# Performance work log

Measured on AMD Instinct MI355X. Metric: run time of the kernel, lower is better.

Reference implementation:

```python
import jax, jax.numpy as jnp
import numpy as np

B, C, H, W = 32, 64, 56, 56
M, DIM, HEADS = 6, 192, 8
INNER = HEADS * C  # 512


def setup_inputs() -> dict:
    key = jax.random.key(0)
    ks = jax.random.split(key, 8)
    s = lambda fan: 1.0 / np.sqrt(fan)
    return {
        "x": jax.random.normal(ks[0], (B, C, H, W), jnp.float32),
        "z": jax.random.normal(ks[1], (B, M, DIM), jnp.float32),
        "Wk": jax.random.normal(ks[2], (DIM, INNER), jnp.float32) * s(DIM),
        "bk": jax.random.normal(ks[3], (INNER,), jnp.float32) * 0.01,
        "Wv": jax.random.normal(ks[4], (DIM, INNER), jnp.float32) * s(DIM),
        "bv": jax.random.normal(ks[5], (INNER,), jnp.float32) * 0.01,
        "Wo": jax.random.normal(ks[6], (INNER, C), jnp.float32) * s(INNER),
        "bo": jax.random.normal(ks[7], (C,), jnp.float32) * 0.01,
    }


def reference(x, z, Wk, bk, Wv, bv, Wo, bo):
    b, c, h, w = x.shape
    m = z.shape[1]
    heads = Wk.shape[1] // c
    scale = c ** (-0.5)
    # shared query: [b, hw, c] (broadcast over heads)
    q = x.reshape(b, c, h * w).transpose(0, 2, 1)
    # NOTE: original uses .view(b, heads, m, c) on [b, m, heads*c] -> pure reshape (no transpose)
    k = (z @ Wk + bk).reshape(b, heads, m, c)
    v = (z @ Wv + bv).reshape(b, heads, m, c)
    dots = jnp.einsum('bnc,bhmc->bhnm', q, k) * scale  # [b, heads, hw, m]
    attn = jax.nn.softmax(dots, axis=-1)
    out = jnp.einsum('bhnm,bhmc->bhnc', attn, v)       # [b, heads, hw, c]
    res = out.transpose(0, 2, 1, 3).reshape(b, h * w, heads * c)
    out = res @ Wo + bo                                 # [b, hw, c] (dropout: eval mode, identity)
    # NOTE: original does .view(b, c, h, w) on [b, hw, c] -> pure reshape (no transpose)
    out = out.reshape(b, c, h, w)
    return out + x
```

## Files before the change

kernel.cpp:

```cpp
#include <hip/hip_runtime.h>
#include <math.h>

#define NB 32
#define NC 64
#define NHW 3136
#define NM 6
#define NDIM 192
#define NHEADS 8
#define NINNER 512
#define NKV 3072
#define CHW (NC * NHW)
#define NG 48

__global__ __launch_bounds__(256) void kv_proj_kernel(
    const float* __restrict__ z, const float* __restrict__ Wk,
    const float* __restrict__ bk, const float* __restrict__ Wv,
    const float* __restrict__ bv, const float* __restrict__ Wo,
    float* __restrict__ kt, float* __restrict__ vw) {
  const int b = blockIdx.x;
  const int chunk = blockIdx.y;
  const int tid = threadIdx.x;
  const int idx = chunk * 256 + tid;
  const int mtok = chunk >> 1;
  const int i = idx & 511;

  __shared__ float vs[256];

  const float* __restrict__ zr = z + b * (NM * NDIM) + mtok * NDIM;

  float ak0 = bk[i], ak1 = 0.f, av0 = bv[i], av1 = 0.f;
  #pragma unroll 8
  for (int d = 0; d < NDIM; d += 2) {
    const float z0 = zr[d], z1 = zr[d + 1];
    ak0 = fmaf(z0, Wk[d * NINNER + i], ak0);
    ak1 = fmaf(z1, Wk[(d + 1) * NINNER + i], ak1);
    av0 = fmaf(z0, Wv[d * NINNER + i], av0);
    av1 = fmaf(z1, Wv[(d + 1) * NINNER + i], av1);
  }
  {
    const int h2 = idx / 384;
    const int mm2 = (idx >> 6) % 6;
    const int cc2 = idx & 63;
    kt[b * NKV + h2 * (NC * NM) + cc2 * NM + mm2] = ak0 + ak1;
  }
  vs[tid] = av0 + av1;
  __syncthreads();

  const int gl = tid >> 6;
  const int c = tid & 63;
  const int g = chunk * 4 + gl;
  const int h = g / 6;
  float a0 = 0.f, a1 = 0.f;
  #pragma unroll 8
  for (int cc = 0; cc < NC; cc += 2) {
    a0 = fmaf(vs[gl * 64 + cc],     Wo[(h * NC + cc) * NC + c],     a0);
    a1 = fmaf(vs[gl * 64 + cc + 1], Wo[(h * NC + cc + 1) * NC + c], a1);
  }
  vw[b * NKV + g * NC + c] = a0 + a1;
}

__global__ __launch_bounds__(512, 4) void attn_kernel(
    const float* __restrict__ x, const float* __restrict__ kt,
    const float* __restrict__ vw, const float* __restrict__ bo,
    float* __restrict__ out) {
  const int b = blockIdx.x;
  const int lane = threadIdx.x & 63;
  const int w = __builtin_amdgcn_readfirstlane((int)(threadIdx.x >> 6));
  const int n0 = blockIdx.y * 64;
  const int n = n0 + lane;
  const float* __restrict__ xb = x + (size_t)b * CHW;

  __shared__ float qs[NC][64];
  __shared__ float aw[NG][64];

  {
    const int tc = threadIdx.x >> 4;
    const int tn4 = (threadIdx.x & 15) * 4;
    #pragma unroll
    for (int rep = 0; rep < 2; ++rep) {
      const int c = tc + rep * 32;
      const float4 xv = *(const float4*)(xb + (size_t)c * NHW + n0 + tn4);
      *(float4*)(&qs[c][tn4]) = xv;
    }
  }
  __syncthreads();

  const float* __restrict__ kh = kt + b * NKV + w * (NC * NM);

  float d[NM];
  #pragma unroll
  for (int mm = 0; mm < NM; ++mm) d[mm] = 0.f;

  #pragma unroll 8
  for (int cc = 0; cc < NC; ++cc) {
    const float qv = qs[cc][lane];
    #pragma unroll
    for (int mm = 0; mm < NM; ++mm)
      d[mm] = fmaf(qv, kh[cc * NM + mm], d[mm]);
  }

  const float scale = 0.125f;
  {
    float mx = d[0];
    #pragma unroll
    for (int mm = 1; mm < NM; ++mm) mx = fmaxf(mx, d[mm]);
    float e[NM], s = 0.f;
    #pragma unroll
    for (int mm = 0; mm < NM; ++mm) { e[mm] = __expf((d[mm] - mx) * scale); s += e[mm]; }
    const float r = 1.0f / s;
    #pragma unroll
    for (int mm = 0; mm < NM; ++mm) aw[w * NM + mm][lane] = e[mm] * r;
  }
  __syncthreads();

  const int c0 = w * 8;
  const float* __restrict__ vb = vw + b * NKV + c0;
  float4 o0 = {0, 0, 0, 0}, o1 = {0, 0, 0, 0};

  #pragma unroll 4
  for (int g = 0; g < NG; ++g) {
    const float a = aw[g][lane];
    const float4 v0 = *(const float4*)(vb + g * NC);
    const float4 v1 = *(const float4*)(vb + g * NC + 4);
    o0.x = fmaf(a, v0.x, o0.x); o0.y = fmaf(a, v0.y, o0.y);
    o0.z = fmaf(a, v0.z, o0.z); o0.w = fmaf(a, v0.w, o0.w);
    o1.x = fmaf(a, v1.x, o1.x); o1.y = fmaf(a, v1.y, o1.y);
    o1.z = fmaf(a, v1.z, o1.z); o1.w = fmaf(a, v1.w, o1.w);
  }

  const size_t base = (size_t)b * CHW + (size_t)n * NC + c0;
  const float4* __restrict__ xr = (const float4*)(x + base);
  const float4 b0 = *(const float4*)(bo + c0);
  const float4 b1 = *(const float4*)(bo + c0 + 4);
  const float4 x0 = xr[0];
  const float4 x1 = xr[1];
  float4 r0, r1;
  r0.x = o0.x + b0.x + x0.x; r0.y = o0.y + b0.y + x0.y;
  r0.z = o0.z + b0.z + x0.z; r0.w = o0.w + b0.w + x0.w;
  r1.x = o1.x + b1.x + x1.x; r1.y = o1.y + b1.y + x1.y;
  r1.z = o1.z + b1.z + x1.z; r1.w = o1.w + b1.w + x1.w;

  float4* __restrict__ op = (float4*)(out + base);
  op[0] = r0;
  op[1] = r1;
}

extern "C" void kernel_launch(void* const* d_in, const int* in_sizes, int n_in,
                              void* d_out, int out_size, void* d_ws, size_t ws_size,
                              hipStream_t stream) {
  const float* x  = (const float*)d_in[0];
  const float* z  = (const float*)d_in[1];
  const float* Wk = (const float*)d_in[2];
  const float* bk = (const float*)d_in[3];
  const float* Wv = (const float*)d_in[4];
  const float* bv = (const float*)d_in[5];
  const float* Wo = (const float*)d_in[6];
  const float* bo = (const float*)d_in[7];
  float* out = (float*)d_out;

  float* ws = (float*)d_ws;
  float* kt = ws;
  float* vw = ws + NB * NKV;

  kv_proj_kernel<<<dim3(NB, 12), 256, 0, stream>>>(z, Wk, bk, Wv, bv, Wo,
                                                   kt, vw);
  attn_kernel<<<dim3(NB, 49), 512, 0, stream>>>(x, kt, vw, bo, out);
}
```

Before: 119.7 us.

## Split-K the KV projection across 4 waves and process two tiles per attention block

The KV projection kernel now uses 1024 threads per block. Each group of 256 threads reduces a quarter of the 192-long dot product, and the partial sums are combined through shared memory, which shortens the serial FMA chain. The attention kernel now loops over two 64-pixel tiles per block and halves its grid. This amortizes the per-block setup and the bias loads, but it adds a barrier per tile and reduces parallelism in the memory-bound main kernel.

```diff
diff --git a/kernel.cpp b/kernel.cpp
--- a/kernel.cpp
+++ b/kernel.cpp
@@ -12,7 +12,7 @@
 #define CHW (NC * NHW)
 #define NG 48
 
-__global__ __launch_bounds__(256) void kv_proj_kernel(
+__global__ __launch_bounds__(1024) void kv_proj_kernel(
     const float* __restrict__ z, const float* __restrict__ Wk,
     const float* __restrict__ bk, const float* __restrict__ Wv,
     const float* __restrict__ bv, const float* __restrict__ Wo,
@@ -20,43 +20,56 @@
   const int b = blockIdx.x;
   const int chunk = blockIdx.y;
   const int tid = threadIdx.x;
-  const int idx = chunk * 256 + tid;
+  const int u = tid & 255;
+  const int s = __builtin_amdgcn_readfirstlane(tid >> 8);
+  const int idx = chunk * 256 + u;
   const int mtok = chunk >> 1;
   const int i = idx & 511;
 
+  __shared__ float kp[1024];
+  __shared__ float vp[1024];
   __shared__ float vs[256];
 
   const float* __restrict__ zr = z + b * (NM * NDIM) + mtok * NDIM;
 
-  float ak0 = bk[i], ak1 = 0.f, av0 = bv[i], av1 = 0.f;
+  float ak0 = 0.f, ak1 = 0.f, av0 = 0.f, av1 = 0.f;
+  const int dlo = s * 48;
   #pragma unroll 8
-  for (int d = 0; d < NDIM; d += 2) {
+  for (int d = dlo; d < dlo + 48; d += 2) {
     const float z0 = zr[d], z1 = zr[d + 1];
     ak0 = fmaf(z0, Wk[d * NINNER + i], ak0);
     ak1 = fmaf(z1, Wk[(d + 1) * NINNER + i], ak1);
     av0 = fmaf(z0, Wv[d * NINNER + i], av0);
     av1 = fmaf(z1, Wv[(d + 1) * NINNER + i], av1);
   }
-  {
+  kp[tid] = ak0 + ak1;
+  vp[tid] = av0 + av1;
+  __syncthreads();
+
+  if (tid < 256) {
+    const float kf = bk[i] + ((kp[u] + kp[256 + u]) + (kp[512 + u] + kp[768 + u]));
+    const float vf = bv[i] + ((vp[u] + vp[256 + u]) + (vp[512 + u] + vp[768 + u]));
     const int h2 = idx / 384;
     const int mm2 = (idx >> 6) % 6;
     const int cc2 = idx & 63;
-    kt[b * NKV + h2 * (NC * NM) + cc2 * NM + mm2] = ak0 + ak1;
+    kt[b * NKV + h2 * (NC * NM) + cc2 * NM + mm2] = kf;
+    vs[u] = vf;
   }
-  vs[tid] = av0 + av1;
   __syncthreads();
 
-  const int gl = tid >> 6;
-  const int c = tid & 63;
-  const int g = chunk * 4 + gl;
-  const int h = g / 6;
-  float a0 = 0.f, a1 = 0.f;
-  #pragma unroll 8
-  for (int cc = 0; cc < NC; cc += 2) {
-    a0 = fmaf(vs[gl * 64 + cc],     Wo[(h * NC + cc) * NC + c],     a0);
-    a1 = fmaf(vs[gl * 64 + cc + 1], Wo[(h * NC + cc + 1) * NC + c], a1);
+  if (tid < 256) {
+    const int gl = u >> 6;
+    const int c = u & 63;
+    const int g = chunk * 4 + gl;
+    const int h = g / 6;
+    float a0 = 0.f, a1 = 0.f;
+    #pragma unroll 8
+    for (int cc = 0; cc < NC; cc += 2) {
+      a0 = fmaf(vs[gl * 64 + cc],     Wo[(h * NC + cc) * NC + c],     a0);
+      a1 = fmaf(vs[gl * 64 + cc + 1], Wo[(h * NC + cc + 1) * NC + c], a1);
+    }
+    vw[b * NKV + g * NC + c] = a0 + a1;
   }
-  vw[b * NKV + g * NC + c] = a0 + a1;
 }
 
 __global__ __launch_bounds__(512, 4) void attn_kernel(
@@ -66,83 +79,93 @@
   const int b = blockIdx.x;
   const int lane = threadIdx.x & 63;
   const int w = __builtin_amdgcn_readfirstlane((int)(threadIdx.x >> 6));
-  const int n0 = blockIdx.y * 64;
-  const int n = n0 + lane;
   const float* __restrict__ xb = x + (size_t)b * CHW;
 
   __shared__ float qs[NC][64];
   __shared__ float aw[NG][64];
 
-  {
-    const int tc = threadIdx.x >> 4;
-    const int tn4 = (threadIdx.x & 15) * 4;
-    #pragma unroll
-    for (int rep = 0; rep < 2; ++rep) {
-      const int c = tc + rep * 32;
-      const float4 xv = *(const float4*)(xb + (size_t)c * NHW + n0 + tn4);
-      *(float4*)(&qs[c][tn4]) = xv;
-    }
-  }
-  __syncthreads();
-
   const float* __restrict__ kh = kt + b * NKV + w * (NC * NM);
-
-  float d[NM];
-  #pragma unroll
-  for (int mm = 0; mm < NM; ++mm) d[mm] = 0.f;
-
-  #pragma unroll 8
-  for (int cc = 0; cc < NC; ++cc) {
-    const float qv = qs[cc][lane];
-    #pragma unroll
-    for (int mm = 0; mm < NM; ++mm)
-      d[mm] = fmaf(qv, kh[cc * NM + mm], d[mm]);
-  }
-
-  const float scale = 0.125f;
-  {
-    float mx = d[0];
-    #pragma unroll
-    for (int mm = 1; mm < NM; ++mm) mx = fmaxf(mx, d[mm]);
-    float e[NM], s = 0.f;
-    #pragma unroll
-    for (int mm = 0; mm < NM; ++mm) { e[mm] = __expf((d[mm] - mx) * scale); s += e[mm]; }
-    const float r = 1.0f / s;
-    #pragma unroll
-    for (int mm = 0; mm < NM; ++mm) aw[w * NM + mm][lane] = e[mm] * r;
-  }
-  __syncthreads();
-
   const int c0 = w * 8;
   const float* __restrict__ vb = vw + b * NKV + c0;
-  float4 o0 = {0, 0, 0, 0}, o1 = {0, 0, 0, 0};
+  const float4 bo0 = *(const float4*)(bo + c0);
+  const float4 bo1 = *(const float4*)(bo + c0 + 4);
+  const float scale = 0.125f;
 
-  #pragma unroll 4
-  for (int g = 0; g < NG; ++g) {
-    const float a = aw[g][lane];
-    const float4 v0 = *(const float4*)(vb + g * NC);
-    const float4 v1 = *(const float4*)(vb + g * NC + 4);
-    o0.x = fmaf(a, v0.x, o0.x); o0.y = fmaf(a, v0.y, o0.y);
-    o0.z = fmaf(a, v0.z, o0.z); o0.w = fmaf(a, v0.w, o0.w);
-    o1.x = fmaf(a, v1.x, o1.x); o1.y = fmaf(a, v1.y, o1.y);
-    o1.z = fmaf(a, v1.z, o1.z); o1.w = fmaf(a, v1.w, o1.w);
+  #pragma unroll 1
+  for (int rep = 0; rep < 2; ++rep) {
+    const int tile = blockIdx.y * 2 + rep;
+    if (tile < 49) {
+      const int n0 = tile * 64;
+
+      {
+        const int tc = threadIdx.x >> 4;
+        const int tn4 = (threadIdx.x & 15) * 4;
+        #pragma unroll
+        for (int r2 = 0; r2 < 2; ++r2) {
+          const int c = tc + r2 * 32;
+          *(float4*)(&qs[c][tn4]) =
+              *(const float4*)(xb + (size_t)c * NHW + n0 + tn4);
+        }
+      }
+      __syncthreads();
+
+      float d[NM];
+      #pragma unroll
+      for (int mm = 0; mm < NM; ++mm) d[mm] = 0.f;
+
+      #pragma unroll 8
+      for (int cc = 0; cc < NC; ++cc) {
+        const float qv = qs[cc][lane];
+        #pragma unroll
+        for (int mm = 0; mm < NM; ++mm)
+          d[mm] = fmaf(qv, kh[cc * NM + mm], d[mm]);
+      }
+
+      {
+        float mx = d[0];
+        #pragma unroll
+        for (int mm = 1; mm < NM; ++mm) mx = fmaxf(mx, d[mm]);
+        float e[NM], ssum = 0.f;
+        #pragma unroll
+        for (int mm = 0; mm < NM; ++mm) {
+          e[mm] = __expf((d[mm] - mx) * scale);
+          ssum += e[mm];
+        }
+        const float r = 1.0f / ssum;
+        #pragma unroll
+        for (int mm = 0; mm < NM; ++mm) aw[w * NM + mm][lane] = e[mm] * r;
+      }
+      __syncthreads();
+
+      float4 o0 = {0, 0, 0, 0}, o1 = {0, 0, 0, 0};
+      #pragma unroll 4
+      for (int g = 0; g < NG; ++g) {
+        const float a = aw[g][lane];
+        const float4 v0 = *(const float4*)(vb + g * NC);
+        const float4 v1 = *(const float4*)(vb + g * NC + 4);
+        o0.x = fmaf(a, v0.x, o0.x); o0.y = fmaf(a, v0.y, o0.y);
+        o0.z = fmaf(a, v0.z, o0.z); o0.w = fmaf(a, v0.w, o0.w);
+        o1.x = fmaf(a, v1.x, o1.x); o1.y = fmaf(a, v1.y, o1.y);
+        o1.z = fmaf(a, v1.z, o1.z); o1.w = fmaf(a, v1.w, o1.w);
+      }
+
+      const int n = n0 + lane;
+      const size_t base = (size_t)b * CHW + (size_t)n * NC + c0;
+      const float4* __restrict__ xr = (const float4*)(x + base);
+      const float4 x0 = xr[0];
+      const float4 x1 = xr[1];
+      float4 r0, r1;
+      r0.x = o0.x + bo0.x + x0.x; r0.y = o0.y + bo0.y + x0.y;
+      r0.z = o0.z + bo0.z + x0.z; r0.w = o0.w + bo0.w + x0.w;
+      r1.x = o1.x + bo1.x + x1.x; r1.y = o1.y + bo1.y + x1.y;
+      r1.z = o1.z + bo1.z + x1.z; r1.w = o1.w + bo1.w + x1.w;
+
+      float4* __restrict__ op = (float4*)(out + base);
+      op[0] = r0;
+      op[1] = r1;
+    }
+    __syncthreads();
   }
-
-  const size_t base = (size_t)b * CHW + (size_t)n * NC + c0;
-  const float4* __restrict__ xr = (const float4*)(x + base);
-  const float4 b0 = *(const float4*)(bo + c0);
-  const float4 b1 = *(const float4*)(bo + c0 + 4);
-  const float4 x0 = xr[0];
-  const float4 x1 = xr[1];
-  float4 r0, r1;
-  r0.x = o0.x + b0.x + x0.x; r0.y = o0.y + b0.y + x0.y;
-  r0.z = o0.z + b0.z + x0.z; r0.w = o0.w + b0.w + x0.w;
-  r1.x = o1.x + b1.x + x1.x; r1.y = o1.y + b1.y + x1.y;
-  r1.z = o1.z + b1.z + x1.z; r1.w = o1.w + b1.w + x1.w;
-
-  float4* __restrict__ op = (float4*)(out + base);
-  op[0] = r0;
-  op[1] = r1;
 }
 
 extern "C" void kernel_launch(void* const* d_in, const int* in_sizes, int n_in,
@@ -162,7 +185,7 @@
   float* kt = ws;
   float* vw = ws + NB * NKV;
 
-  kv_proj_kernel<<<dim3(NB, 12), 256, 0, stream>>>(z, Wk, bk, Wv, bv, Wo,
-                                                   kt, vw);
-  attn_kernel<<<dim3(NB, 49), 512, 0, stream>>>(x, kt, vw, bo, out);
+  kv_proj_kernel<<<dim3(NB, 12), 1024, 0, stream>>>(z, Wk, bk, Wv, bv, Wo,
+                                                    kt, vw);
+  attn_kernel<<<dim3(NB, 25), 512, 0, stream>>>(x, kt, vw, bo, out);
 }
```

After: 120.7 us. About the same (+0.8%).
